# Kernel tuning notes

Hardware: AMD Instinct MI355X
Metric: run time of the kernel (lower is better)

The kernel has to match this reference:

```python
import jax, jax.numpy as jnp
import numpy as np

DIM = 1024
HIDDEN = 2816  # multiple_of * ceil(int(2*4096/3)/multiple_of)
N_MODALITIES = 2
B, S = 8, 4096


def setup_inputs() -> dict:
    key = jax.random.key(0)
    k_x, k_m, k1, k2, k3 = jax.random.split(key, 5)
    x = jax.random.normal(k_x, (B, S, DIM), dtype=jnp.float32)
    modality_ids = jax.random.randint(k_m, (B, S), 0, N_MODALITIES, dtype=jnp.int32)
    in_std = DIM ** -0.5
    out_std = HIDDEN ** -0.5
    # Linear weight layout: [out_features, in_features], stacked over modalities.
    W1 = jax.random.normal(k1, (N_MODALITIES, HIDDEN, DIM), dtype=jnp.float32) * in_std
    W3 = jax.random.normal(k3, (N_MODALITIES, HIDDEN, DIM), dtype=jnp.float32) * in_std
    W2 = jax.random.normal(k2, (N_MODALITIES, DIM, HIDDEN), dtype=jnp.float32) * out_std
    return {"x": x, "modality_ids": modality_ids, "W1": W1, "W2": W2, "W3": W3}


def reference(x, modality_ids, W1, W2, W3):
    # Masked per-modality SwiGLU; equivalent to gather -> expert MLP -> scatter.
    output = jnp.zeros_like(x)
    for m in range(N_MODALITIES):  # small fixed modality count
        mask = (modality_ids == m)[..., None]          # [B, S, 1]
        x1 = jnp.einsum('bsd,hd->bsh', x, W1[m])       # gate proj
        x3 = jnp.einsum('bsd,hd->bsh', x, W3[m])       # up proj
        out_m = jnp.einsum('bsh,dh->bsd', jax.nn.silu(x1) * x3, W2[m])
        output = output + jnp.where(mask, out_m, 0.0)
    return output
```

## Files before the change

### kernel.cpp

```cpp
#include <hip/hip_runtime.h>
#include <stdint.h>

#define DIMK 1024
#define HID  2816
#define BM   128
#define BN   128
#define BK   64

typedef __attribute__((ext_vector_type(8))) __bf16 bf16x8;
typedef __attribute__((ext_vector_type(4))) float  f32x4;

typedef const __attribute__((address_space(1))) void* gas1_t;
typedef __attribute__((address_space(3))) void*       las3_t;

__device__ __forceinline__ uint16_t f2bf(float f) {
  uint32_t u = __float_as_uint(f);
  u += 0x7FFFu + ((u >> 16) & 1u);
  return (uint16_t)(u >> 16);
}

__device__ __forceinline__ void gload16(const uint16_t* g, uint16_t* l) {
  __builtin_amdgcn_global_load_lds((gas1_t)g, (las3_t)l, 16, 0, 0);
}

__device__ __forceinline__ void stage_tile(const uint16_t* g, long rowStride, uint16_t* l, int tid) {
  const int wv = tid >> 6, lane = tid & 63;
  const int r  = lane >> 3;
  const int cb = (lane & 7) * 8;
#pragma unroll
  for (int i = 0; i < 4; ++i) {
    const int seg = wv * 4 + i;
    gload16(g + (long)(seg * 8 + r) * rowStride + cb, l + seg * 512 + lane * 8);
  }
}


__global__ void count_kernel(const int* __restrict__ mids, int* __restrict__ bc, int T) {
  const int b = blockIdx.x, t = threadIdx.x;
  const int token = b * 256 + t;
  const int lane = t & 63, wv = t >> 6;
  const int m = (token < T) ? mids[token] : -1;
  unsigned long long m0 = __ballot(m == 0);
  unsigned long long m1 = __ballot(m == 1);
  __shared__ int w0[4], w1[4];
  if (lane == 0) { w0[wv] = __popcll(m0); w1[wv] = __popcll(m1); }
  __syncthreads();
  if (t == 0) {
    bc[2 * b]     = w0[0] + w0[1] + w0[2] + w0[3];
    bc[2 * b + 1] = w1[0] + w1[1] + w1[2] + w1[3];
  }
}

__global__ void scan_kernel(const int* __restrict__ bc, int* __restrict__ base,
                            int* __restrict__ counters, int nb) {
  __shared__ int s0[256], s1[256];
  const int t = threadIdx.x;
  const int v0 = (t < nb) ? bc[2 * t] : 0;
  const int v1 = (t < nb) ? bc[2 * t + 1] : 0;
  s0[t] = v0; s1[t] = v1;
  __syncthreads();
  for (int off = 1; off < 256; off <<= 1) {
    int a0 = (t >= off) ? s0[t - off] : 0;
    int a1 = (t >= off) ? s1[t - off] : 0;
    __syncthreads();
    s0[t] += a0; s1[t] += a1;
    __syncthreads();
  }
  if (t < nb) { base[2 * t] = s0[t] - v0; base[2 * t + 1] = s1[t] - v1; }
  if (t == nb - 1) { counters[0] = s0[t]; counters[1] = s1[t]; }
}

__global__ void slot_kernel(const int* __restrict__ mids, const int* __restrict__ base,
                            const int* __restrict__ counters, int* __restrict__ tok,
                            int* __restrict__ slotof, int T) {
  const int b = blockIdx.x, t = threadIdx.x;
  const int token = b * 256 + t;
  const int lane = t & 63, wv = t >> 6;
  const int m = (token < T) ? mids[token] : -1;
  unsigned long long m0 = __ballot(m == 0);
  unsigned long long m1 = __ballot(m == 1);
  __shared__ int w0[4], w1[4];
  if (lane == 0) { w0[wv] = __popcll(m0); w1[wv] = __popcll(m1); }
  __syncthreads();
  int pre0 = 0, pre1 = 0;
  for (int w = 0; w < wv; ++w) { pre0 += w0[w]; pre1 += w1[w]; }
  if (token >= T) return;
  const unsigned long long below = (1ULL << lane) - 1ULL;
  const int c0 = counters[0];
  const int al0 = ((c0 + 127) >> 7) << 7;
  int slot;
  if (m == 0) slot = base[2 * b] + pre0 + __popcll(m0 & below);
  else        slot = al0 + base[2 * b + 1] + pre1 + __popcll(m1 & below);
  tok[slot] = token;
  slotof[token] = slot;
}

__global__ void copy_kernel(const float* __restrict__ x, const int* __restrict__ slotof,
                            uint16_t* __restrict__ xg, int T) {
  const int token = blockIdx.x * 4 + (threadIdx.x >> 6);
  if (token >= T) return;
  const int lane = threadIdx.x & 63;
  const int slot = slotof[token];
  const float4* src = (const float4*)(x + (long)token * DIMK);
  uint16_t* dst = xg + (long)slot * DIMK;
#pragma unroll
  for (int j = 0; j < 4; ++j) {
    float4 v = src[lane + 64 * j];
    ushort4 o;
    o.x = f2bf(v.x); o.y = f2bf(v.y); o.z = f2bf(v.z); o.w = f2bf(v.w);
    *(ushort4*)(dst + (lane + 64 * j) * 4) = o;
  }
}

__global__ void convert_kernel(const float* __restrict__ src, uint16_t* __restrict__ dst, long n) {
  long i = ((long)blockIdx.x * blockDim.x + threadIdx.x) * 4;
  if (i >= n) return;
  float4 v = *(const float4*)(src + i);
  ushort4 o;
  o.x = f2bf(v.x); o.y = f2bf(v.y); o.z = f2bf(v.z); o.w = f2bf(v.w);
  *(ushort4*)(dst + i) = o;
}

__global__ __launch_bounds__(256, 2) void gemm1_kernel(
    const uint16_t* __restrict__ xg, const uint16_t* __restrict__ w1b,
    const uint16_t* __restrict__ w3b, uint16_t* __restrict__ hbuf,
    const int* __restrict__ counters) {
  __shared__ __align__(16) uint16_t lsA[BM * BK];
  __shared__ __align__(16) uint16_t lsB1[BM * BK];
  __shared__ __align__(16) uint16_t lsB3[BM * BK];

  const int c0 = counters[0], c1 = counters[1];
  const int t0 = (c0 + 127) >> 7, t1 = (c1 + 127) >> 7;
  const int rt = blockIdx.x;
  if (rt >= t0 + t1) return;
  const int mod  = (rt < t0) ? 0 : 1;
  const int row0 = rt * BM;
  const int ht   = blockIdx.y;

  const int tid = threadIdx.x;
  const int lane = tid & 63, wv = tid >> 6;
  const int wr = wv >> 1, wc = wv & 1;
  const int lrow = lane & 15, lk = (lane >> 4) * 8;

  const uint16_t* gA  = xg  + (long)row0 * DIMK;
  const uint16_t* gB1 = w1b + ((long)mod * HID + ht * BN) * DIMK;
  const uint16_t* gB3 = w3b + ((long)mod * HID + ht * BN) * DIMK;

  f32x4 accG[4][4], accU[4][4];
#pragma unroll
  for (int m = 0; m < 4; ++m)
#pragma unroll
    for (int n = 0; n < 4; ++n) {
      accG[m][n] = {0.f, 0.f, 0.f, 0.f};
      accU[m][n] = {0.f, 0.f, 0.f, 0.f};
    }

  for (int kt = 0; kt < DIMK / BK; ++kt) {
    stage_tile(gA  + kt * BK, DIMK, lsA,  tid);
    stage_tile(gB1 + kt * BK, DIMK, lsB1, tid);
    stage_tile(gB3 + kt * BK, DIMK, lsB3, tid);
    asm volatile("s_waitcnt vmcnt(0)" ::: "memory");
    __syncthreads();
#pragma unroll
    for (int ks = 0; ks < 2; ++ks) {
      bf16x8 a[4], b1[4], b3[4];
#pragma unroll
      for (int m = 0; m < 4; ++m)
        a[m] = *reinterpret_cast<const bf16x8*>(&lsA[(wr * 64 + m * 16 + lrow) * BK + ks * 32 + lk]);
#pragma unroll
      for (int n = 0; n < 4; ++n) {
        b1[n] = *reinterpret_cast<const bf16x8*>(&lsB1[(wc * 64 + n * 16 + lrow) * BK + ks * 32 + lk]);
        b3[n] = *reinterpret_cast<const bf16x8*>(&lsB3[(wc * 64 + n * 16 + lrow) * BK + ks * 32 + lk]);
      }
#pragma unroll
      for (int m = 0; m < 4; ++m)
#pragma unroll
        for (int n = 0; n < 4; ++n) {
          accG[m][n] = __builtin_amdgcn_mfma_f32_16x16x32_bf16(a[m], b1[n], accG[m][n], 0, 0, 0);
          accU[m][n] = __builtin_amdgcn_mfma_f32_16x16x32_bf16(a[m], b3[n], accU[m][n], 0, 0, 0);
        }
    }
    __syncthreads();
  }

#pragma unroll
  for (int m = 0; m < 4; ++m)
#pragma unroll
    for (int n = 0; n < 4; ++n) {
      const int col = ht * BN + wc * 64 + n * 16 + lrow;
#pragma unroll
      for (int i = 0; i < 4; ++i) {
        const int row = row0 + wr * 64 + m * 16 + (lane >> 4) * 4 + i;
        float g = accG[m][n][i];
        float u = accU[m][n][i];
        float hv = (g / (1.f + __expf(-g))) * u;
        hbuf[(long)row * HID + col] = f2bf(hv);
      }
    }
}

__global__ __launch_bounds__(256, 2) void gemm2_kernel(
    const uint16_t* __restrict__ hbuf, const uint16_t* __restrict__ w2b,
    const int* __restrict__ counters, const int* __restrict__ tok,
    float* __restrict__ out) {
  __shared__ __align__(16) uint16_t lsA[BM * BK];
  __shared__ __align__(16) uint16_t lsB[BM * BK];

  const int c0 = counters[0], c1 = counters[1];
  const int t0 = (c0 + 127) >> 7, t1 = (c1 + 127) >> 7;
  const int rt = blockIdx.x;
  if (rt >= t0 + t1) return;
  const int mod  = (rt < t0) ? 0 : 1;
  const int row0 = rt * BM;
  const int ct   = blockIdx.y;
  const int vlimit = (mod == 0) ? c0 : t0 * BM + c1;

  const int tid = threadIdx.x;
  const int lane = tid & 63, wv = tid >> 6;
  const int wr = wv >> 1, wc = wv & 1;
  const int lrow = lane & 15, lk = (lane >> 4) * 8;

  const uint16_t* gA = hbuf + (long)row0 * HID;
  const uint16_t* gB = w2b + ((long)mod * DIMK + ct * BN) * HID;

  f32x4 acc[4][4];
#pragma unroll
  for (int m = 0; m < 4; ++m)
#pragma unroll
    for (int n = 0; n < 4; ++n) acc[m][n] = {0.f, 0.f, 0.f, 0.f};

  for (int kt = 0; kt < HID / BK; ++kt) {
    stage_tile(gA + kt * BK, HID, lsA, tid);
    stage_tile(gB + kt * BK, HID, lsB, tid);
    asm volatile("s_waitcnt vmcnt(0)" ::: "memory");
    __syncthreads();
#pragma unroll
    for (int ks = 0; ks < 2; ++ks) {
      bf16x8 a[4], b[4];
#pragma unroll
      for (int m = 0; m < 4; ++m)
        a[m] = *reinterpret_cast<const bf16x8*>(&lsA[(wr * 64 + m * 16 + lrow) * BK + ks * 32 + lk]);
#pragma unroll
      for (int n = 0; n < 4; ++n)
        b[n] = *reinterpret_cast<const bf16x8*>(&lsB[(wc * 64 + n * 16 + lrow) * BK + ks * 32 + lk]);
#pragma unroll
      for (int m = 0; m < 4; ++m)
#pragma unroll
        for (int n = 0; n < 4; ++n)
          acc[m][n] = __builtin_amdgcn_mfma_f32_16x16x32_bf16(a[m], b[n], acc[m][n], 0, 0, 0);
    }
    __syncthreads();
  }

#pragma unroll
  for (int m = 0; m < 4; ++m)
#pragma unroll
    for (int n = 0; n < 4; ++n) {
      const int col = ct * BN + wc * 64 + n * 16 + lrow;
#pragma unroll
      for (int i = 0; i < 4; ++i) {
        const int row = row0 + wr * 64 + m * 16 + (lane >> 4) * 4 + i;
        if (row < vlimit) {
          int t = tok[row];
          out[(long)t * DIMK + col] = acc[m][n][i];
        }
      }
    }
}

extern "C" void kernel_launch(void* const* d_in, const int* in_sizes, int n_in,
                              void* d_out, int out_size, void* d_ws, size_t ws_size,
                              hipStream_t stream) {
  const float* x    = (const float*)d_in[0];
  const int*   mids = (const int*)d_in[1];
  const float* W1   = (const float*)d_in[2];
  const float* W2   = (const float*)d_in[3];
  const float* W3   = (const float*)d_in[4];
  float* out = (float*)d_out;

  const int T   = in_sizes[1];
  const int NB  = (T + 255) / 256;
  const int CAP = ((T + 127) / 128) * 128 + 128;

  char* ws = (char*)d_ws;
  int* counters = (int*)ws;
  int* bc   = (int*)(ws + 256);
  int* base = (int*)(ws + 256 + 2048);
  int* tok  = (int*)(ws + 256 + 4096);
  int* slotof = tok + ((CAP + 63) & ~63);
  size_t off = 256 + 4096 + (size_t)((CAP + 63) & ~63) * 4 + (size_t)((T + 63) & ~63) * 4;
  off = (off + 255) & ~(size_t)255;
  uint16_t* xg  = (uint16_t*)(ws + off); off += (size_t)CAP * DIMK * 2;
  uint16_t* w1b = (uint16_t*)(ws + off); off += (size_t)2 * HID * DIMK * 2;
  uint16_t* w3b = (uint16_t*)(ws + off); off += (size_t)2 * HID * DIMK * 2;
  uint16_t* w2b = (uint16_t*)(ws + off); off += (size_t)2 * DIMK * HID * 2;
  uint16_t* hbuf = (uint16_t*)(ws + off); off += (size_t)CAP * HID * 2;
  (void)ws_size; (void)n_in; (void)out_size;

  count_kernel<<<NB, 256, 0, stream>>>(mids, bc, T);
  scan_kernel<<<1, 256, 0, stream>>>(bc, base, counters, NB);
  slot_kernel<<<NB, 256, 0, stream>>>(mids, base, counters, tok, slotof, T);
  copy_kernel<<<(T + 3) / 4, 256, 0, stream>>>(x, slotof, xg, T);

  const long NW = (long)2 * HID * DIMK;
  const int cblk = (int)((NW / 4 + 255) / 256);
  convert_kernel<<<cblk, 256, 0, stream>>>(W1, w1b, NW);
  convert_kernel<<<cblk, 256, 0, stream>>>(W3, w3b, NW);
  convert_kernel<<<cblk, 256, 0, stream>>>(W2, w2b, NW);

  const int rtiles = CAP / BM;
  gemm1_kernel<<<dim3(rtiles, HID / BN), 256, 0, stream>>>(xg, w1b, w3b, hbuf, counters);
  gemm2_kernel<<<dim3(rtiles, DIMK / BN), 256, 0, stream>>>(hbuf, w2b, counters, tok, out);
}
```

Measured before the change: 790.3 us.

## Double-buffer GEMMs with 256-row tiles, swizzled LDS, and XCD-aware block remap

Both GEMM kernels move from 128x128 single-buffered tiles with a full vmcnt(0) wait to 256x128 tiles over 8 waves. They double-buffer LDS and issue next-tile global-to-LDS loads in stages interleaved with the MFMA phases, using partial vmcnt waits and setprio. LDS rows are XOR-swizzled to avoid bank conflicts, and the block index is remapped so neighbouring tiles land on the same XCD for L2 reuse. Modality row padding grows to 256, which adds some padded rows of wasted work and uses more LDS per block, possibly lowering occupancy.

```diff
diff --git a/kernel.cpp b/kernel.cpp
--- a/kernel.cpp
+++ b/kernel.cpp
@@ -3,9 +3,6 @@
 
 #define DIMK 1024
 #define HID  2816
-#define BM   128
-#define BN   128
-#define BK   64
 
 typedef __attribute__((ext_vector_type(8))) __bf16 bf16x8;
 typedef __attribute__((ext_vector_type(4))) float  f32x4;
@@ -23,15 +20,26 @@
   __builtin_amdgcn_global_load_lds((gas1_t)g, (las3_t)l, 16, 0, 0);
 }
 
-__device__ __forceinline__ void stage_tile(const uint16_t* g, long rowStride, uint16_t* l, int tid) {
-  const int wv = tid >> 6, lane = tid & 63;
-  const int r  = lane >> 3;
-  const int cb = (lane & 7) * 8;
-#pragma unroll
-  for (int i = 0; i < 4; ++i) {
-    const int seg = wv * 4 + i;
-    gload16(g + (long)(seg * 8 + r) * rowStride + cb, l + seg * 512 + lane * 8);
-  }
+template<int N> __device__ __forceinline__ void wait_vm() {
+  if constexpr (N == 0)      asm volatile("s_waitcnt vmcnt(0)" ::: "memory");
+  else if constexpr (N == 2) asm volatile("s_waitcnt vmcnt(2)" ::: "memory");
+  else                       asm volatile("s_waitcnt vmcnt(4)" ::: "memory");
+}
+
+__device__ __forceinline__ void stage_half(const uint16_t* g, long stride,
+                                           uint16_t* lds, int wv, int lane) {
+  const int rsub = lane >> 3;
+  const int gsw  = ((lane & 7) ^ rsub) << 3;
+#pragma unroll
+  for (int j = 0; j < 2; ++j) {
+    const int blk = j * 8 + wv;
+    gload16(g + (long)(blk * 8 + rsub) * stride + gsw,
+            lds + blk * 512 + lane * 8);
+  }
+}
+
+__device__ __forceinline__ bf16x8 ldsf(const uint16_t* lds, int r, int g) {
+  return *reinterpret_cast<const bf16x8*>(lds + r * 64 + ((g ^ (r & 7)) << 3));
 }
 
 
@@ -87,7 +95,7 @@
   if (token >= T) return;
   const unsigned long long below = (1ULL << lane) - 1ULL;
   const int c0 = counters[0];
-  const int al0 = ((c0 + 127) >> 7) << 7;
+  const int al0 = ((c0 + 255) >> 8) << 8;
   int slot;
   if (m == 0) slot = base[2 * b] + pre0 + __popcll(m0 & below);
   else        slot = al0 + base[2 * b + 1] + pre1 + __popcll(m1 & below);
@@ -121,148 +129,287 @@
   *(ushort4*)(dst + i) = o;
 }
 
-__global__ __launch_bounds__(256, 2) void gemm1_kernel(
+
+template<bool PF, int W0, int W1, int W2>
+__device__ __forceinline__ void g1_tile(
+    const uint16_t* Ac, const uint16_t* B1c, const uint16_t* B3c,
+    uint16_t* An, uint16_t* B1n, uint16_t* B3n,
+    const uint16_t* gA, const uint16_t* gB1, const uint16_t* gB3, long ko,
+    int wv, int lane, int wr, int wc, int lrow, int grp,
+    f32x4 (&accG)[8][2], f32x4 (&accU)[8][2]) {
+  bf16x8 a[4][2], b1[2][2], b3[2][2];
+  wait_vm<W0>();
+  __builtin_amdgcn_s_barrier();
+  asm volatile("" ::: "memory");
+#pragma unroll
+  for (int m = 0; m < 4; ++m)
+#pragma unroll
+    for (int ks = 0; ks < 2; ++ks)
+      a[m][ks] = ldsf(Ac, m * 32 + wr * 16 + lrow, ks * 4 + grp);
+#pragma unroll
+  for (int n = 0; n < 2; ++n)
+#pragma unroll
+    for (int ks = 0; ks < 2; ++ks)
+      b1[n][ks] = ldsf(B1c, wc * 32 + n * 16 + lrow, ks * 4 + grp);
+  if constexpr (PF) stage_half(gA + ko, DIMK, An, wv, lane);
+  asm volatile("s_waitcnt lgkmcnt(0)" ::: "memory");
+  __builtin_amdgcn_sched_barrier(0);
+  __builtin_amdgcn_s_setprio(1);
+#pragma unroll
+  for (int ks = 0; ks < 2; ++ks)
+#pragma unroll
+    for (int m = 0; m < 4; ++m)
+#pragma unroll
+      for (int n = 0; n < 2; ++n)
+        accG[m][n] = __builtin_amdgcn_mfma_f32_16x16x32_bf16(a[m][ks], b1[n][ks], accG[m][n], 0, 0, 0);
+  __builtin_amdgcn_s_setprio(0);
+  wait_vm<W1>();
+  __builtin_amdgcn_s_barrier();
+  asm volatile("" ::: "memory");
+#pragma unroll
+  for (int n = 0; n < 2; ++n)
+#pragma unroll
+    for (int ks = 0; ks < 2; ++ks)
+      b3[n][ks] = ldsf(B3c, wc * 32 + n * 16 + lrow, ks * 4 + grp);
+  if constexpr (PF) stage_half(gB1 + ko, DIMK, B1n, wv, lane);
+  asm volatile("s_waitcnt lgkmcnt(0)" ::: "memory");
+  __builtin_amdgcn_sched_barrier(0);
+  __builtin_amdgcn_s_setprio(1);
+#pragma unroll
+  for (int ks = 0; ks < 2; ++ks)
+#pragma unroll
+    for (int m = 0; m < 4; ++m)
+#pragma unroll
+      for (int n = 0; n < 2; ++n)
+        accU[m][n] = __builtin_amdgcn_mfma_f32_16x16x32_bf16(a[m][ks], b3[n][ks], accU[m][n], 0, 0, 0);
+  __builtin_amdgcn_s_setprio(0);
+  wait_vm<W2>();
+  __builtin_amdgcn_s_barrier();
+  asm volatile("" ::: "memory");
+#pragma unroll
+  for (int m = 0; m < 4; ++m)
+#pragma unroll
+    for (int ks = 0; ks < 2; ++ks)
+      a[m][ks] = ldsf(Ac, (m + 4) * 32 + wr * 16 + lrow, ks * 4 + grp);
+  if constexpr (PF) stage_half(gB3 + ko, DIMK, B3n, wv, lane);
+  asm volatile("s_waitcnt lgkmcnt(0)" ::: "memory");
+  __builtin_amdgcn_sched_barrier(0);
+  __builtin_amdgcn_s_setprio(1);
+#pragma unroll
+  for (int ks = 0; ks < 2; ++ks)
+#pragma unroll
+    for (int m = 0; m < 4; ++m)
+#pragma unroll
+      for (int n = 0; n < 2; ++n)
+        accG[m + 4][n] = __builtin_amdgcn_mfma_f32_16x16x32_bf16(a[m][ks], b1[n][ks], accG[m + 4][n], 0, 0, 0);
+  __builtin_amdgcn_s_setprio(0);
+  if constexpr (PF) stage_half(gA + 128 * DIMK + ko, DIMK, An + 128 * 64, wv, lane);
+  __builtin_amdgcn_s_setprio(1);
+#pragma unroll
+  for (int ks = 0; ks < 2; ++ks)
+#pragma unroll
+    for (int m = 0; m < 4; ++m)
+#pragma unroll
+      for (int n = 0; n < 2; ++n)
+        accU[m + 4][n] = __builtin_amdgcn_mfma_f32_16x16x32_bf16(a[m][ks], b3[n][ks], accU[m + 4][n], 0, 0, 0);
+  __builtin_amdgcn_s_setprio(0);
+}
+
+__global__ __launch_bounds__(512, 2) void gemm1_kernel(
     const uint16_t* __restrict__ xg, const uint16_t* __restrict__ w1b,
     const uint16_t* __restrict__ w3b, uint16_t* __restrict__ hbuf,
     const int* __restrict__ counters) {
-  __shared__ __align__(16) uint16_t lsA[BM * BK];
-  __shared__ __align__(16) uint16_t lsB1[BM * BK];
-  __shared__ __align__(16) uint16_t lsB3[BM * BK];
+  __shared__ __align__(16) uint16_t lsA[2][256 * 64];
+  __shared__ __align__(16) uint16_t lsB1[2][128 * 64];
+  __shared__ __align__(16) uint16_t lsB3[2][128 * 64];
 
   const int c0 = counters[0], c1 = counters[1];
-  const int t0 = (c0 + 127) >> 7, t1 = (c1 + 127) >> 7;
-  const int rt = blockIdx.x;
+  const int t0 = (c0 + 255) >> 8, t1 = (c1 + 255) >> 8;
+  const int GX = gridDim.x;
+  const int nwg = GX * (int)gridDim.y;
+  const int orig = blockIdx.y * GX + blockIdx.x;
+  const int q = nwg >> 3, r = nwg & 7;
+  const int xcd = orig & 7, loc = orig >> 3;
+  const int swz = (xcd < r ? xcd * (q + 1) : r * (q + 1) + (xcd - r) * q) + loc;
+  const int ht = swz / GX;
+  const int rt = swz - ht * GX;
   if (rt >= t0 + t1) return;
-  const int mod  = (rt < t0) ? 0 : 1;
-  const int row0 = rt * BM;
-  const int ht   = blockIdx.y;
-
-  const int tid = threadIdx.x;
-  const int lane = tid & 63, wv = tid >> 6;
-  const int wr = wv >> 1, wc = wv & 1;
-  const int lrow = lane & 15, lk = (lane >> 4) * 8;
-
-  const uint16_t* gA  = xg  + (long)row0 * DIMK;
-  const uint16_t* gB1 = w1b + ((long)mod * HID + ht * BN) * DIMK;
-  const uint16_t* gB3 = w3b + ((long)mod * HID + ht * BN) * DIMK;
-
-  f32x4 accG[4][4], accU[4][4];
-#pragma unroll
-  for (int m = 0; m < 4; ++m)
-#pragma unroll
-    for (int n = 0; n < 4; ++n) {
+  const int mod = (rt < t0) ? 0 : 1;
+  const long row0 = (long)rt * 256;
+
+  const int tid = threadIdx.x, lane = tid & 63, wv = tid >> 6;
+  const int wr = wv >> 2, wc = wv & 3;
+  const int lrow = lane & 15, grp = lane >> 4;
+
+  const uint16_t* gA  = xg  + row0 * DIMK;
+  const uint16_t* gB1 = w1b + ((long)mod * HID + ht * 128) * DIMK;
+  const uint16_t* gB3 = w3b + ((long)mod * HID + ht * 128) * DIMK;
+
+  f32x4 accG[8][2], accU[8][2];
+#pragma unroll
+  for (int m = 0; m < 8; ++m)
+#pragma unroll
+    for (int n = 0; n < 2; ++n) {
       accG[m][n] = {0.f, 0.f, 0.f, 0.f};
       accU[m][n] = {0.f, 0.f, 0.f, 0.f};
     }
 
-  for (int kt = 0; kt < DIMK / BK; ++kt) {
-    stage_tile(gA  + kt * BK, DIMK, lsA,  tid);
-    stage_tile(gB1 + kt * BK, DIMK, lsB1, tid);
-    stage_tile(gB3 + kt * BK, DIMK, lsB3, tid);
-    asm volatile("s_waitcnt vmcnt(0)" ::: "memory");
-    __syncthreads();
-#pragma unroll
-    for (int ks = 0; ks < 2; ++ks) {
-      bf16x8 a[4], b1[4], b3[4];
-#pragma unroll
-      for (int m = 0; m < 4; ++m)
-        a[m] = *reinterpret_cast<const bf16x8*>(&lsA[(wr * 64 + m * 16 + lrow) * BK + ks * 32 + lk]);
-#pragma unroll
-      for (int n = 0; n < 4; ++n) {
-        b1[n] = *reinterpret_cast<const bf16x8*>(&lsB1[(wc * 64 + n * 16 + lrow) * BK + ks * 32 + lk]);
-        b3[n] = *reinterpret_cast<const bf16x8*>(&lsB3[(wc * 64 + n * 16 + lrow) * BK + ks * 32 + lk]);
-      }
-#pragma unroll
-      for (int m = 0; m < 4; ++m)
-#pragma unroll
-        for (int n = 0; n < 4; ++n) {
-          accG[m][n] = __builtin_amdgcn_mfma_f32_16x16x32_bf16(a[m], b1[n], accG[m][n], 0, 0, 0);
-          accU[m][n] = __builtin_amdgcn_mfma_f32_16x16x32_bf16(a[m], b3[n], accU[m][n], 0, 0, 0);
-        }
-    }
-    __syncthreads();
-  }
-
-#pragma unroll
-  for (int m = 0; m < 4; ++m)
-#pragma unroll
-    for (int n = 0; n < 4; ++n) {
-      const int col = ht * BN + wc * 64 + n * 16 + lrow;
+  stage_half(gA,             DIMK, &lsA[0][0],        wv, lane);
+  stage_half(gB1,            DIMK, &lsB1[0][0],       wv, lane);
+  stage_half(gB3,            DIMK, &lsB3[0][0],       wv, lane);
+  stage_half(gA + 128 * DIMK, DIMK, &lsA[0][128 * 64], wv, lane);
+
+  const int NT = DIMK / 64;
+  int cur = 0;
+  for (int t = 0; t < NT - 1; ++t) {
+    g1_tile<true, 4, 4, 4>(&lsA[cur][0], &lsB1[cur][0], &lsB3[cur][0],
+                           &lsA[cur ^ 1][0], &lsB1[cur ^ 1][0], &lsB3[cur ^ 1][0],
+                           gA, gB1, gB3, (long)(t + 1) * 64,
+                           wv, lane, wr, wc, lrow, grp, accG, accU);
+    cur ^= 1;
+  }
+  g1_tile<false, 4, 2, 0>(&lsA[cur][0], &lsB1[cur][0], &lsB3[cur][0],
+                          &lsA[cur ^ 1][0], &lsB1[cur ^ 1][0], &lsB3[cur ^ 1][0],
+                          gA, gB1, gB3, 0,
+                          wv, lane, wr, wc, lrow, grp, accG, accU);
+
+#pragma unroll
+  for (int m = 0; m < 8; ++m)
+#pragma unroll
+    for (int n = 0; n < 2; ++n) {
+      const int col = ht * 128 + wc * 32 + n * 16 + lrow;
 #pragma unroll
       for (int i = 0; i < 4; ++i) {
-        const int row = row0 + wr * 64 + m * 16 + (lane >> 4) * 4 + i;
+        const long row = row0 + m * 32 + wr * 16 + grp * 4 + i;
         float g = accG[m][n][i];
         float u = accU[m][n][i];
         float hv = (g / (1.f + __expf(-g))) * u;
-        hbuf[(long)row * HID + col] = f2bf(hv);
+        hbuf[row * HID + col] = f2bf(hv);
       }
     }
 }
 
-__global__ __launch_bounds__(256, 2) void gemm2_kernel(
+
+template<bool PF, int W0, int W1>
+__device__ __forceinline__ void g2_tile(
+    const uint16_t* Ac, const uint16_t* Bc, uint16_t* An, uint16_t* Bn,
+    const uint16_t* gA, const uint16_t* gB, long ko,
+    int wv, int lane, int wr, int wc, int lrow, int grp,
+    f32x4 (&acc)[8][2]) {
+  bf16x8 a[4][2], b[2][2];
+  wait_vm<W0>();
+  __builtin_amdgcn_s_barrier();
+  asm volatile("" ::: "memory");
+#pragma unroll
+  for (int m = 0; m < 4; ++m)
+#pragma unroll
+    for (int ks = 0; ks < 2; ++ks)
+      a[m][ks] = ldsf(Ac, m * 32 + wr * 16 + lrow, ks * 4 + grp);
+#pragma unroll
+  for (int n = 0; n < 2; ++n)
+#pragma unroll
+    for (int ks = 0; ks < 2; ++ks)
+      b[n][ks] = ldsf(Bc, wc * 32 + n * 16 + lrow, ks * 4 + grp);
+  if constexpr (PF) {
+    stage_half(gA + ko, HID, An, wv, lane);
+    stage_half(gB + ko, HID, Bn, wv, lane);
+  }
+  asm volatile("s_waitcnt lgkmcnt(0)" ::: "memory");
+  __builtin_amdgcn_sched_barrier(0);
+  __builtin_amdgcn_s_setprio(1);
+#pragma unroll
+  for (int ks = 0; ks < 2; ++ks)
+#pragma unroll
+    for (int m = 0; m < 4; ++m)
+#pragma unroll
+      for (int n = 0; n < 2; ++n)
+        acc[m][n] = __builtin_amdgcn_mfma_f32_16x16x32_bf16(a[m][ks], b[n][ks], acc[m][n], 0, 0, 0);
+  __builtin_amdgcn_s_setprio(0);
+  wait_vm<W1>();
+  __builtin_amdgcn_s_barrier();
+  asm volatile("" ::: "memory");
+#pragma unroll
+  for (int m = 0; m < 4; ++m)
+#pragma unroll
+    for (int ks = 0; ks < 2; ++ks)
+      a[m][ks] = ldsf(Ac, (m + 4) * 32 + wr * 16 + lrow, ks * 4 + grp);
+  if constexpr (PF) stage_half(gA + 128 * HID + ko, HID, An + 128 * 64, wv, lane);
+  asm volatile("s_waitcnt lgkmcnt(0)" ::: "memory");
+  __builtin_amdgcn_sched_barrier(0);
+  __builtin_amdgcn_s_setprio(1);
+#pragma unroll
+  for (int ks = 0; ks < 2; ++ks)
+#pragma unroll
+    for (int m = 0; m < 4; ++m)
+#pragma unroll
+      for (int n = 0; n < 2; ++n)
+        acc[m + 4][n] = __builtin_amdgcn_mfma_f32_16x16x32_bf16(a[m][ks], b[n][ks], acc[m + 4][n], 0, 0, 0);
+  __builtin_amdgcn_s_setprio(0);
+}
+
+__global__ __launch_bounds__(512, 2) void gemm2_kernel(
     const uint16_t* __restrict__ hbuf, const uint16_t* __restrict__ w2b,
     const int* __restrict__ counters, const int* __restrict__ tok,
     float* __restrict__ out) {
-  __shared__ __align__(16) uint16_t lsA[BM * BK];
-  __shared__ __align__(16) uint16_t lsB[BM * BK];
+  __shared__ __align__(16) uint16_t lsA[2][256 * 64];
+  __shared__ __align__(16) uint16_t lsB[2][128 * 64];
 
   const int c0 = counters[0], c1 = counters[1];
-  const int t0 = (c0 + 127) >> 7, t1 = (c1 + 127) >> 7;
-  const int rt = blockIdx.x;
+  const int t0 = (c0 + 255) >> 8, t1 = (c1 + 255) >> 8;
+  const int GX = gridDim.x;
+  const int nwg = GX * (int)gridDim.y;
+  const int orig = blockIdx.y * GX + blockIdx.x;
+  const int q = nwg >> 3, r = nwg & 7;
+  const int xcd = orig & 7, loc = orig >> 3;
+  const int swz = (xcd < r ? xcd * (q + 1) : r * (q + 1) + (xcd - r) * q) + loc;
+  const int ct = swz / GX;
+  const int rt = swz - ct * GX;
   if (rt >= t0 + t1) return;
-  const int mod  = (rt < t0) ? 0 : 1;
-  const int row0 = rt * BM;
-  const int ct   = blockIdx.y;
-  const int vlimit = (mod == 0) ? c0 : t0 * BM + c1;
-
-  const int tid = threadIdx.x;
-  const int lane = tid & 63, wv = tid >> 6;
-  const int wr = wv >> 1, wc = wv & 1;
-  const int lrow = lane & 15, lk = (lane >> 4) * 8;
-
-  const uint16_t* gA = hbuf + (long)row0 * HID;
-  const uint16_t* gB = w2b + ((long)mod * DIMK + ct * BN) * HID;
-
-  f32x4 acc[4][4];
-#pragma unroll
-  for (int m = 0; m < 4; ++m)
-#pragma unroll
-    for (int n = 0; n < 4; ++n) acc[m][n] = {0.f, 0.f, 0.f, 0.f};
-
-  for (int kt = 0; kt < HID / BK; ++kt) {
-    stage_tile(gA + kt * BK, HID, lsA, tid);
-    stage_tile(gB + kt * BK, HID, lsB, tid);
-    asm volatile("s_waitcnt vmcnt(0)" ::: "memory");
-    __syncthreads();
-#pragma unroll
-    for (int ks = 0; ks < 2; ++ks) {
-      bf16x8 a[4], b[4];
-#pragma unroll
-      for (int m = 0; m < 4; ++m)
-        a[m] = *reinterpret_cast<const bf16x8*>(&lsA[(wr * 64 + m * 16 + lrow) * BK + ks * 32 + lk]);
-#pragma unroll
-      for (int n = 0; n < 4; ++n)
-        b[n] = *reinterpret_cast<const bf16x8*>(&lsB[(wc * 64 + n * 16 + lrow) * BK + ks * 32 + lk]);
-#pragma unroll
-      for (int m = 0; m < 4; ++m)
-#pragma unroll
-        for (int n = 0; n < 4; ++n)
-          acc[m][n] = __builtin_amdgcn_mfma_f32_16x16x32_bf16(a[m], b[n], acc[m][n], 0, 0, 0);
-    }
-    __syncthreads();
-  }
-
-#pragma unroll
-  for (int m = 0; m < 4; ++m)
-#pragma unroll
-    for (int n = 0; n < 4; ++n) {
-      const int col = ct * BN + wc * 64 + n * 16 + lrow;
+  const int mod = (rt < t0) ? 0 : 1;
+  const long row0 = (long)rt * 256;
+  const int vlimit = (mod == 0) ? c0 : t0 * 256 + c1;
+
+  const int tid = threadIdx.x, lane = tid & 63, wv = tid >> 6;
+  const int wr = wv >> 2, wc = wv & 3;
+  const int lrow = lane & 15, grp = lane >> 4;
+
+  const uint16_t* gA = hbuf + row0 * HID;
+  const uint16_t* gB = w2b + ((long)mod * DIMK + ct * 128) * HID;
+
+  f32x4 acc[8][2];
+#pragma unroll
+  for (int m = 0; m < 8; ++m)
+#pragma unroll
+    for (int n = 0; n < 2; ++n) acc[m][n] = {0.f, 0.f, 0.f, 0.f};
+
+  stage_half(gA,             HID, &lsA[0][0],        wv, lane);
+  stage_half(gB,             HID, &lsB[0][0],        wv, lane);
+  stage_half(gA + 128 * HID, HID, &lsA[0][128 * 64], wv, lane);
+
+  const int NT = HID / 64;
+  int cur = 0;
+  for (int t = 0; t < NT - 1; ++t) {
+    g2_tile<true, 2, 4>(&lsA[cur][0], &lsB[cur][0],
+                        &lsA[cur ^ 1][0], &lsB[cur ^ 1][0],
+                        gA, gB, (long)(t + 1) * 64,
+                        wv, lane, wr, wc, lrow, grp, acc);
+    cur ^= 1;
+  }
+  g2_tile<false, 2, 0>(&lsA[cur][0], &lsB[cur][0],
+                       &lsA[cur ^ 1][0], &lsB[cur ^ 1][0],
+                       gA, gB, 0,
+                       wv, lane, wr, wc, lrow, grp, acc);
+
+#pragma unroll
+  for (int m = 0; m < 8; ++m)
+#pragma unroll
+    for (int n = 0; n < 2; ++n) {
+      const int col = ct * 128 + wc * 32 + n * 16 + lrow;
 #pragma unroll
       for (int i = 0; i < 4; ++i) {
-        const int row = row0 + wr * 64 + m * 16 + (lane >> 4) * 4 + i;
+        const int row = (int)row0 + m * 32 + wr * 16 + grp * 4 + i;
         if (row < vlimit) {
-          int t = tok[row];
-          out[(long)t * DIMK + col] = acc[m][n][i];
+          out[(long)tok[row] * DIMK + col] = acc[m][n][i];
         }
       }
     }
@@ -280,7 +427,7 @@
 
   const int T   = in_sizes[1];
   const int NB  = (T + 255) / 256;
-  const int CAP = ((T + 127) / 128) * 128 + 128;
+  const int CAP = ((T + 255) & ~255) + 256;
 
   char* ws = (char*)d_ws;
   int* counters = (int*)ws;
@@ -308,7 +455,7 @@
   convert_kernel<<<cblk, 256, 0, stream>>>(W3, w3b, NW);
   convert_kernel<<<cblk, 256, 0, stream>>>(W2, w2b, NW);
 
-  const int rtiles = CAP / BM;
-  gemm1_kernel<<<dim3(rtiles, HID / BN), 256, 0, stream>>>(xg, w1b, w3b, hbuf, counters);
-  gemm2_kernel<<<dim3(rtiles, DIMK / BN), 256, 0, stream>>>(hbuf, w2b, counters, tok, out);
-}
+  const int rtiles = CAP / 256;
+  gemm1_kernel<<<dim3(rtiles, HID / 128), 512, 0, stream>>>(xg, w1b, w3b, hbuf, counters);
+  gemm2_kernel<<<dim3(rtiles, DIMK / 128), 512, 0, stream>>>(hbuf, w2b, counters, tok, out);
+}
```

Measured after the change: 772.9 us. -2.2%, faster.
